# Optimization experiments

Hardware: AMD Instinct MI355X
Metric: run time of the kernel (lower is better)

## Reference

```python
import jax, jax.numpy as jnp
import numpy as np

N_NODES = 25000
N_EDGES = 300000
B = 25            # graphs in the batch
NPG = N_NODES // B
D = 128           # hidden_dim == out_dim
H = 8             # num_heads
HD = D // H
L = 4             # num_layers
VOCAB = 30000
N_ETYPE = 8


def setup_inputs() -> dict:
    key = jax.random.key(0)
    ks = jax.random.split(key, 16)
    s = 0.05
    # graph structure: edges kept within each graph
    eg = jax.random.randint(ks[0], (N_EDGES,), 0, B)
    src = eg * NPG + jax.random.randint(ks[1], (N_EDGES,), 0, NPG)
    dst = eg * NPG + jax.random.randint(ks[2], (N_EDGES,), 0, NPG)
    tokens = jax.random.randint(ks[3], (N_NODES,), 0, VOCAB)
    etype = jax.random.randint(ks[4], (N_EDGES,), 0, N_ETYPE)
    graph_id = jnp.arange(N_NODES) // NPG
    return {
        "emb_h": jax.random.normal(ks[5], (VOCAB, D)) * s,
        "emb_e": jax.random.normal(ks[6], (N_ETYPE, D)) * s,
        # per-layer stacked params: Q,K,V,proj_e weights (bias=False)
        "w_qkve": jax.random.normal(ks[7], (L, 4, D, D)) * s,
        # output projections O_h, O_e
        "o_w": jax.random.normal(ks[8], (L, 2, D, D)) * s,
        "o_b": jnp.zeros((L, 2, D)),
        # layernorms: [ln1_h, ln1_e, ln2_h, ln2_e]
        "ln_scale": jnp.ones((L, 4, D)),
        "ln_bias": jnp.zeros((L, 4, D)),
        # FFNs for h and e: D -> 2D -> D
        "ffn_w1": jax.random.normal(ks[9], (L, 2, D, 2 * D)) * s,
        "ffn_b1": jnp.zeros((L, 2, 2 * D)),
        "ffn_w2": jax.random.normal(ks[10], (L, 2, 2 * D, D)) * s,
        "ffn_b2": jnp.zeros((L, 2, D)),
        # MLPReadout (L=2): 128 -> 64 -> 32 -> 1
        "mlp_w0": jax.random.normal(ks[11], (D, D // 2)) * s,
        "mlp_b0": jnp.zeros((D // 2,)),
        "mlp_w1": jax.random.normal(ks[12], (D // 2, D // 4)) * s,
        "mlp_b1": jnp.zeros((D // 4,)),
        "mlp_w2": jax.random.normal(ks[13], (D // 4, 1)) * s,
        "mlp_b2": jnp.zeros((1,)),
        "tokens": tokens,
        "etype": etype,
        "src": src,
        "dst": dst,
        "graph_id": graph_id,
    }


def _ln(x, g, b):
    m = jnp.mean(x, axis=-1, keepdims=True)
    v = jnp.mean(jnp.square(x - m), axis=-1, keepdims=True)
    return g * (x - m) / jnp.sqrt(v + 1e-5) + b


def _layer(h, e, src, dst, wq, wk, wv, we, o_w, o_b, ln_s, ln_b,
           ffn_w1, ffn_b1, ffn_w2, ffn_b2):
    n = h.shape[0]
    Q = (h @ wq).reshape(n, H, HD)
    K = (h @ wk).reshape(n, H, HD)
    V = (h @ wv).reshape(n, H, HD)
    pe = (e @ we).reshape(-1, H, HD)
    # per-edge implicit attention: (K_src * Q_dst)/sqrt(d) * proj_e
    score = (K[src] * Q[dst]) / jnp.sqrt(jnp.asarray(HD, h.dtype)) * pe  # [E,H,HD]
    e_att = score.reshape(-1, D)
    w = jnp.exp(jnp.clip(jnp.sum(score, axis=-1, keepdims=True), -5.0, 5.0))  # [E,H,1]
    wV = jax.ops.segment_sum((V[src] * w).reshape(-1, D), dst, num_segments=n)
    z = jax.ops.segment_sum(w[:, :, 0], dst, num_segments=n)  # [N,H]
    h_att = (wV.reshape(n, H, HD) / (z[:, :, None] + 1e-6)).reshape(n, D)
    # O proj + residual + LN
    h1 = _ln(h + (h_att @ o_w[0] + o_b[0]), ln_s[0], ln_b[0])
    e1 = _ln(e + (e_att @ o_w[1] + o_b[1]), ln_s[1], ln_b[1])
    # FFNs + residual + LN
    h2 = _ln(h1 + jax.nn.relu(h1 @ ffn_w1[0] + ffn_b1[0]) @ ffn_w2[0] + ffn_b2[0],
             ln_s[2], ln_b[2])
    e2 = _ln(e1 + jax.nn.relu(e1 @ ffn_w1[1] + ffn_b1[1]) @ ffn_w2[1] + ffn_b2[1],
             ln_s[3], ln_b[3])
    return h2, e2


def reference(emb_h, emb_e, w_qkve, o_w, o_b, ln_scale, ln_bias,
              ffn_w1, ffn_b1, ffn_w2, ffn_b2,
              mlp_w0, mlp_b0, mlp_w1, mlp_b1, mlp_w2, mlp_b2,
              tokens, etype, src, dst, graph_id):
    h = emb_h[tokens]   # [N,D]
    e = emb_e[etype]    # [E,D]
    for l in range(L):
        h, e = _layer(h, e, src, dst,
                      w_qkve[l, 0], w_qkve[l, 1], w_qkve[l, 2], w_qkve[l, 3],
                      o_w[l], o_b[l], ln_scale[l], ln_bias[l],
                      ffn_w1[l], ffn_b1[l], ffn_w2[l], ffn_b2[l])
    # mean-nodes readout per graph
    hg_sum = jax.ops.segment_sum(h, graph_id, num_segments=B)
    cnt = jax.ops.segment_sum(jnp.ones((h.shape[0], 1), h.dtype), graph_id, num_segments=B)
    hg = hg_sum / cnt
    # MLPReadout
    y = jax.nn.relu(hg @ mlp_w0 + mlp_b0)
    y = jax.nn.relu(y @ mlp_w1 + mlp_b1)
    return y @ mlp_w2 + mlp_b2  # [B,1]
```

## Files before the change

### kernel.cpp

```cpp
#include <hip/hip_runtime.h>
#include <cstdint>

#define NN 25000
#define NE 300000

typedef unsigned short ushort_t;
typedef __attribute__((ext_vector_type(8))) short bf16x8;
typedef __attribute__((ext_vector_type(4))) float f32x4;
typedef __attribute__((ext_vector_type(4))) unsigned short u16x4;
typedef __attribute__((ext_vector_type(8))) unsigned short u16x8;

__device__ __forceinline__ float4 ld4(const float* p){ return *reinterpret_cast<const float4*>(p); }
__device__ __forceinline__ void st4(float* p, const float4& v){ *reinterpret_cast<float4*>(p) = v; }
__device__ __forceinline__ float bf2f(ushort_t u){ return __uint_as_float((unsigned)u << 16); }
__device__ __forceinline__ ushort_t f2bfu(float f){
  unsigned x = __float_as_uint(f);
  return (ushort_t)((x + 0x7fffu + ((x >> 16) & 1u)) >> 16);
}

#define FXS 4294967296.0
#define FXI 2.3283064365386963e-10
__device__ __forceinline__ long long f2fx(float v) {
  return (long long)llrint((double)v * FXS);
}
__device__ __forceinline__ float fx2f(long long q) { return (float)((double)q * FXI); }

#define MFMA(a, b, c) __builtin_amdgcn_mfma_f32_16x16x32_bf16((a), (b), (c), 0, 0, 0)

__global__ __launch_bounds__(256)
void wconv_k(const float* __restrict__ src, ushort_t* __restrict__ dst,
             int K, int N, int total)
{
  int i = blockIdx.x * 256 + threadIdx.x;
  if (i >= total) return;
  int kn = K * N;
  int mat = i / kn, r = i - mat * kn;
  int n = r / K, k = r - n * K;
  dst[i] = f2bfu(src[(size_t)mat * kn + (size_t)k * N + n]);
}

__global__ __launch_bounds__(256)
void gather_h_k(const float* __restrict__ tab, const int* __restrict__ idx,
                float* __restrict__ hf, ushort_t* __restrict__ hb)
{
  int t = blockIdx.x * 256 + threadIdx.x;
  if (t >= NN * 32) return;
  int i = t >> 5, c4 = t & 31;
  float4 v = ld4(tab + (size_t)idx[i] * 128 + c4 * 4);
  st4(hf + (size_t)i * 128 + c4 * 4, v);
  u16x4 b = { f2bfu(v.x), f2bfu(v.y), f2bfu(v.z), f2bfu(v.w) };
  *reinterpret_cast<u16x4*>(hb + (size_t)i * 128 + c4 * 4) = b;
}

__global__ __launch_bounds__(256)
void gather_e_k(const float* __restrict__ tab, const int* __restrict__ idx,
                ushort_t* __restrict__ eb)
{
  int t = blockIdx.x * 256 + threadIdx.x;
  if (t >= NE * 32) return;
  int i = t >> 5, c4 = t & 31;
  float4 v = ld4(tab + (size_t)idx[i] * 128 + c4 * 4);
  u16x4 b = { f2bfu(v.x), f2bfu(v.y), f2bfu(v.z), f2bfu(v.w) };
  *reinterpret_cast<u16x4*>(eb + (size_t)i * 128 + c4 * 4) = b;
}

__global__ __launch_bounds__(256)
void count_k(const int* __restrict__ dst, int* __restrict__ counts)
{
  int e = blockIdx.x * 256 + threadIdx.x;
  if (e < NE) atomicAdd(&counts[dst[e]], 1);
}

__global__ __launch_bounds__(1024)
void scan_k(const int* __restrict__ counts, int* __restrict__ start,
            int* __restrict__ cursor)
{
  __shared__ int part[1024];
  const int t = threadIdx.x;
  const int base = t * 25;
  int loc[25];
  int s = 0;
#pragma unroll
  for (int i = 0; i < 25; ++i) {
    int n = base + i;
    int c = (n < NN) ? counts[n] : 0;
    loc[i] = s; s += c;
  }
  part[t] = s;
  __syncthreads();
  for (int off = 1; off < 1024; off <<= 1) {
    int v = (t >= off) ? part[t - off] : 0;
    __syncthreads();
    part[t] += v;
    __syncthreads();
  }
  int excl = (t == 0) ? 0 : part[t - 1];
#pragma unroll
  for (int i = 0; i < 25; ++i) {
    int n = base + i;
    if (n < NN) { int v = excl + loc[i]; start[n] = v; cursor[n] = v; }
  }
  if (t == 0) start[NN] = NE;
}

__global__ __launch_bounds__(256)
void scatter_k(const int* __restrict__ src, const int* __restrict__ dst,
               int* __restrict__ cursor, int2* __restrict__ csr_es)
{
  int e = blockIdx.x * 256 + threadIdx.x;
  if (e >= NE) return;
  int pos = atomicAdd(&cursor[dst[e]], 1);
  csr_es[pos] = make_int2(e, src[e]);
}

__global__ __launch_bounds__(256)
void gemmN_bf_k(const ushort_t* __restrict__ A, const ushort_t* __restrict__ WT,
                const int K, const int M, const int ldo,
                const float* __restrict__ Bias, const int osep,
                const float* __restrict__ ResF, const ushort_t* __restrict__ ResB,
                const float* __restrict__ G, const float* __restrict__ Bb,
                ushort_t* __restrict__ OutB, float* __restrict__ OutF)
{
  __shared__ __align__(16) ushort_t SM[2 * 128 * 136];
  __shared__ float mu[128], rs[128];
  ushort_t* Xs = SM;
  ushort_t* Ws = SM + 128 * 136;
  const int tid = threadIdx.x;
  const int m0 = blockIdx.x * 128;
  const int col0 = blockIdx.y * 128;

  const int l = tid & 63, wv = tid >> 6;
  const int lr = l & 15, lk = l >> 4;
  const int mb = (wv & 1) * 64, nb = (wv >> 1) * 64;
  f32x4 acc[4][4];
  const f32x4 zf = {0.f, 0.f, 0.f, 0.f};
#pragma unroll
  for (int mi = 0; mi < 4; ++mi)
#pragma unroll
    for (int ni = 0; ni < 4; ++ni) acc[mi][ni] = zf;

  for (int kc = 0; kc < K; kc += 128) {
    if (kc) __syncthreads();
    for (int c = tid; c < 2048; c += 256) {
      int r = c >> 4, k8 = c & 15;
      bf16x8 v = {};
      if (m0 + r < M)
        v = *reinterpret_cast<const bf16x8*>(A + (size_t)(m0 + r) * K + kc + k8 * 8);
      *reinterpret_cast<bf16x8*>(Xs + r * 136 + k8 * 8) = v;
    }
    for (int c = tid; c < 2048; c += 256) {
      int r = c >> 4, k8 = c & 15;
      *reinterpret_cast<bf16x8*>(Ws + r * 136 + k8 * 8) =
          *reinterpret_cast<const bf16x8*>(WT + (size_t)(col0 + r) * K + kc + k8 * 8);
    }
    __syncthreads();
#pragma unroll
    for (int kt = 0; kt < 4; ++kt) {
      bf16x8 af[4], bw[4];
#pragma unroll
      for (int i = 0; i < 4; ++i)
        af[i] = *reinterpret_cast<const bf16x8*>(Xs + (mb + i * 16 + lr) * 136 + kt * 32 + lk * 8);
#pragma unroll
      for (int i = 0; i < 4; ++i)
        bw[i] = *reinterpret_cast<const bf16x8*>(Ws + (nb + i * 16 + lr) * 136 + kt * 32 + lk * 8);
#pragma unroll
      for (int mi = 0; mi < 4; ++mi)
#pragma unroll
        for (int ni = 0; ni < 4; ++ni)
          acc[mi][ni] = MFMA(af[mi], bw[ni], acc[mi][ni]);
    }
  }

  if (G == nullptr) {
    __syncthreads();
    ushort_t* Rb = SM;
#pragma unroll
    for (int mi = 0; mi < 4; ++mi)
#pragma unroll
      for (int rr = 0; rr < 4; ++rr) {
        int row = mb + mi * 16 + lk * 4 + rr;
#pragma unroll
        for (int ni = 0; ni < 4; ++ni) {
          int col = nb + ni * 16 + lr;
          float v = acc[mi][ni][rr];
          if (Bias) v = fmaxf(v + Bias[col0 + col], 0.f);
          Rb[row * 136 + col] = f2bfu(v);
        }
      }
    __syncthreads();
    ushort_t* ob = OutB + (osep ? (size_t)blockIdx.y * M * 128 : (size_t)col0);
    for (int c = tid; c < 2048; c += 256) {
      int r = c >> 4, k8 = c & 15;
      if (m0 + r < M)
        *reinterpret_cast<u16x8*>(ob + (size_t)(m0 + r) * ldo + k8 * 8) =
            *reinterpret_cast<u16x8*>(Rb + r * 136 + k8 * 8);
    }
    return;
  }

  __syncthreads();
  float* Tf = reinterpret_cast<float*>(SM);
#pragma unroll
  for (int mi = 0; mi < 4; ++mi)
#pragma unroll
    for (int rr = 0; rr < 4; ++rr) {
      int row = mb + mi * 16 + lk * 4 + rr;
      int grow = m0 + row;
#pragma unroll
      for (int ni = 0; ni < 4; ++ni) {
        int col = nb + ni * 16 + lr;
        float t = acc[mi][ni][rr] + Bias[col];
        if (grow < M)
          t += ResF ? ResF[(size_t)grow * 128 + col] : bf2f(ResB[(size_t)grow * 128 + col]);
        Tf[row * 132 + col] = t;
      }
    }
  __syncthreads();
  {
    int r = tid >> 1, jj = tid & 1;
    const float* tp = Tf + r * 132 + jj * 64;
    float s = 0.f;
    for (int c2 = 0; c2 < 64; ++c2) s += tp[c2];
    s += __shfl_xor(s, 1);
    float mean = s * (1.f / 128.f);
    float v = 0.f;
    for (int c2 = 0; c2 < 64; ++c2) { float d = tp[c2] - mean; v += d * d; }
    v += __shfl_xor(v, 1);
    if (jj == 0) { mu[r] = mean; rs[r] = 1.f / sqrtf(v * (1.f / 128.f) + 1e-5f); }
  }
  __syncthreads();
  for (int c = tid; c < 4096; c += 256) {
    int r = c >> 5, c4 = c & 31;
    int grow = m0 + r;
    if (grow >= M) continue;
    float4 t = ld4(Tf + r * 132 + c4 * 4);
    float4 gv = ld4(G + c4 * 4), bv = ld4(Bb + c4 * 4);
    float m = mu[r], ir = rs[r];
    float o0 = gv.x * (t.x - m) * ir + bv.x;
    float o1 = gv.y * (t.y - m) * ir + bv.y;
    float o2 = gv.z * (t.z - m) * ir + bv.z;
    float o3 = gv.w * (t.w - m) * ir + bv.w;
    u16x4 ub = { f2bfu(o0), f2bfu(o1), f2bfu(o2), f2bfu(o3) };
    *reinterpret_cast<u16x4*>(OutB + (size_t)grow * 128 + c4 * 4) = ub;
    if (OutF) st4(OutF + (size_t)grow * 128 + c4 * 4, make_float4(o0, o1, o2, o3));
  }
}

__global__ __launch_bounds__(256)
void ffn_f_k(const ushort_t* __restrict__ Xbf, const float* __restrict__ ResF,
             const ushort_t* __restrict__ W1T, const float* __restrict__ B1,
             const ushort_t* __restrict__ W2T, const float* __restrict__ B2,
             const float* __restrict__ G, const float* __restrict__ Bb,
             ushort_t* __restrict__ OutB, float* __restrict__ OutF, int M)
{
  __shared__ __align__(16) ushort_t SM[8704 + 8704 + 17408];
  __shared__ float mu[64], rs[64];
  ushort_t* Xs   = SM;
  ushort_t* Mid0 = SM + 8704;
  ushort_t* Wst  = SM + 17408;
  const int tid = threadIdx.x;
  const int m0 = blockIdx.x * 64;
  const int l = tid & 63, wv = tid >> 6, lr = l & 15, lk = l >> 4;
  const f32x4 zf = {0.f, 0.f, 0.f, 0.f};

  for (int c = tid; c < 1024; c += 256) {
    int r = c >> 4, k8 = c & 15;
    bf16x8 v = {};
    if (m0 + r < M) v = *reinterpret_cast<const bf16x8*>(Xbf + (size_t)(m0 + r) * 128 + k8 * 8);
    *reinterpret_cast<bf16x8*>(Xs + r * 136 + k8 * 8) = v;
  }
  for (int c = tid; c < 2048; c += 256) {
    int r = c >> 4, k8 = c & 15;
    *reinterpret_cast<bf16x8*>(Wst + r * 136 + k8 * 8) =
        *reinterpret_cast<const bf16x8*>(W1T + (size_t)r * 128 + k8 * 8);
  }
  __syncthreads();

  f32x4 acc2[8];
#pragma unroll
  for (int i = 0; i < 8; ++i) acc2[i] = zf;
  ushort_t rsv[8][4];

  {
    f32x4 a1[8];
#pragma unroll
    for (int i = 0; i < 8; ++i) a1[i] = zf;
#pragma unroll
    for (int kt = 0; kt < 4; ++kt) {
      bf16x8 af = *reinterpret_cast<const bf16x8*>(Xs + (wv * 16 + lr) * 136 + kt * 32 + lk * 8);
#pragma unroll
      for (int ni = 0; ni < 8; ++ni) {
        bf16x8 bw = *reinterpret_cast<const bf16x8*>(Wst + (ni * 16 + lr) * 136 + kt * 32 + lk * 8);
        a1[ni] = MFMA(af, bw, a1[ni]);
      }
    }
#pragma unroll
    for (int ni = 0; ni < 8; ++ni)
#pragma unroll
      for (int rr = 0; rr < 4; ++rr)
        Mid0[(wv * 16 + lk * 4 + rr) * 136 + ni * 16 + lr] =
            f2bfu(fmaxf(a1[ni][rr] + B1[ni * 16 + lr], 0.f));
  }
  __syncthreads();
  for (int c = tid; c < 2048; c += 256) {
    int r = c >> 4, k8 = c & 15;
    *reinterpret_cast<bf16x8*>(Wst + r * 136 + k8 * 8) =
        *reinterpret_cast<const bf16x8*>(W1T + (size_t)(128 + r) * 128 + k8 * 8);
  }
  __syncthreads();
  {
    f32x4 a1[8];
#pragma unroll
    for (int i = 0; i < 8; ++i) a1[i] = zf;
#pragma unroll
    for (int kt = 0; kt < 4; ++kt) {
      bf16x8 af = *reinterpret_cast<const bf16x8*>(Xs + (wv * 16 + lr) * 136 + kt * 32 + lk * 8);
#pragma unroll
      for (int ni = 0; ni < 8; ++ni) {
        bf16x8 bw = *reinterpret_cast<const bf16x8*>(Wst + (ni * 16 + lr) * 136 + kt * 32 + lk * 8);
        a1[ni] = MFMA(af, bw, a1[ni]);
      }
    }
    __syncthreads();
    if (!ResF) {
#pragma unroll
      for (int ni = 0; ni < 8; ++ni)
#pragma unroll
        for (int rr = 0; rr < 4; ++rr)
          rsv[ni][rr] = Xs[(wv * 16 + lk * 4 + rr) * 136 + ni * 16 + lr];
    }
#pragma unroll
    for (int ni = 0; ni < 8; ++ni)
#pragma unroll
      for (int rr = 0; rr < 4; ++rr)
        Xs[(wv * 16 + lk * 4 + rr) * 136 + ni * 16 + lr] =
            f2bfu(fmaxf(a1[ni][rr] + B1[128 + ni * 16 + lr], 0.f));
  }
  __syncthreads();
  for (int c = tid; c < 2048; c += 256) {
    int r = c >> 4, k8 = c & 15;
    *reinterpret_cast<bf16x8*>(Wst + r * 136 + k8 * 8) =
        *reinterpret_cast<const bf16x8*>(W2T + (size_t)r * 256 + k8 * 8);
  }
  __syncthreads();
#pragma unroll
  for (int kt = 0; kt < 4; ++kt) {
    bf16x8 af = *reinterpret_cast<const bf16x8*>(Mid0 + (wv * 16 + lr) * 136 + kt * 32 + lk * 8);
#pragma unroll
    for (int ni = 0; ni < 8; ++ni) {
      bf16x8 bw = *reinterpret_cast<const bf16x8*>(Wst + (ni * 16 + lr) * 136 + kt * 32 + lk * 8);
      acc2[ni] = MFMA(af, bw, acc2[ni]);
    }
  }
  __syncthreads();
  for (int c = tid; c < 2048; c += 256) {
    int r = c >> 4, k8 = c & 15;
    *reinterpret_cast<bf16x8*>(Wst + r * 136 + k8 * 8) =
        *reinterpret_cast<const bf16x8*>(W2T + (size_t)r * 256 + 128 + k8 * 8);
  }
  __syncthreads();
#pragma unroll
  for (int kt = 0; kt < 4; ++kt) {
    bf16x8 af = *reinterpret_cast<const bf16x8*>(Xs + (wv * 16 + lr) * 136 + kt * 32 + lk * 8);
#pragma unroll
    for (int ni = 0; ni < 8; ++ni) {
      bf16x8 bw = *reinterpret_cast<const bf16x8*>(Wst + (ni * 16 + lr) * 136 + kt * 32 + lk * 8);
      acc2[ni] = MFMA(af, bw, acc2[ni]);
    }
  }
  __syncthreads();
  float* Tf = reinterpret_cast<float*>(Wst);
#pragma unroll
  for (int ni = 0; ni < 8; ++ni)
#pragma unroll
    for (int rr = 0; rr < 4; ++rr) {
      int row = wv * 16 + lk * 4 + rr;
      int grow = m0 + row;
      int col = ni * 16 + lr;
      float t = acc2[ni][rr] + B2[col];
      if (ResF) { if (grow < M) t += ResF[(size_t)grow * 128 + col]; }
      else      t += bf2f(rsv[ni][rr]);
      Tf[row * 132 + col] = t;
    }
  __syncthreads();
  {
    int r = tid >> 2, jj = tid & 3;
    const float* tp = Tf + r * 132 + jj * 32;
    float s = 0.f;
    for (int c2 = 0; c2 < 32; ++c2) s += tp[c2];
    s += __shfl_xor(s, 1); s += __shfl_xor(s, 2);
    float mean = s * (1.f / 128.f);
    float v = 0.f;
    for (int c2 = 0; c2 < 32; ++c2) { float d = tp[c2] - mean; v += d * d; }
    v += __shfl_xor(v, 1); v += __shfl_xor(v, 2);
    if (jj == 0) { mu[r] = mean; rs[r] = 1.f / sqrtf(v * (1.f / 128.f) + 1e-5f); }
  }
  __syncthreads();
  for (int c = tid; c < 2048; c += 256) {
    int r = c >> 5, c4 = c & 31;
    int grow = m0 + r;
    if (grow >= M) continue;
    float4 t = ld4(Tf + r * 132 + c4 * 4);
    float4 gv = ld4(G + c4 * 4), bv = ld4(Bb + c4 * 4);
    float m = mu[r], ir = rs[r];
    float o0 = gv.x * (t.x - m) * ir + bv.x;
    float o1 = gv.y * (t.y - m) * ir + bv.y;
    float o2 = gv.z * (t.z - m) * ir + bv.z;
    float o3 = gv.w * (t.w - m) * ir + bv.w;
    u16x4 ub = { f2bfu(o0), f2bfu(o1), f2bfu(o2), f2bfu(o3) };
    *reinterpret_cast<u16x4*>(OutB + (size_t)grow * 128 + c4 * 4) = ub;
    if (OutF) st4(OutF + (size_t)grow * 128 + c4 * 4, make_float4(o0, o1, o2, o3));
  }
}

__global__ __launch_bounds__(256)
void efused_k(ushort_t* __restrict__ Ebuf,
              const ushort_t* __restrict__ Qb, const ushort_t* __restrict__ Kb,
              const int* __restrict__ src, const int* __restrict__ dst,
              float* __restrict__ wbuf,
              const ushort_t* __restrict__ weT,
              const ushort_t* __restrict__ owT, const float* __restrict__ oBias,
              const float* __restrict__ G1, const float* __restrict__ B1n,
              const ushort_t* __restrict__ W1T, const float* __restrict__ fB1,
              const ushort_t* __restrict__ W2T, const float* __restrict__ fB2,
              const float* __restrict__ G2, const float* __restrict__ B2n,
              int M)
{
  __shared__ __align__(16) ushort_t SM[34816];
  __shared__ float mu[64], rs[64];
  ushort_t* Es   = SM;
  ushort_t* Mid0 = SM + 8704;
  ushort_t* Wst  = SM + 17408;
  const int tid = threadIdx.x;
  const int m0 = blockIdx.x * 64;
  const int l = tid & 63, wv = tid >> 6, lr = l & 15, lk = l >> 4;
  const f32x4 zf = {0.f, 0.f, 0.f, 0.f};

  for (int c = tid; c < 1024; c += 256) {
    int r = c >> 4, k8 = c & 15;
    bf16x8 v = {};
    if (m0 + r < M) v = *reinterpret_cast<const bf16x8*>(Ebuf + (size_t)(m0 + r) * 128 + k8 * 8);
    *reinterpret_cast<bf16x8*>(Es + r * 136 + k8 * 8) = v;
  }
  for (int c = tid; c < 2048; c += 256) {
    int r = c >> 4, k8 = c & 15;
    *reinterpret_cast<bf16x8*>(Wst + r * 136 + k8 * 8) =
        *reinterpret_cast<const bf16x8*>(weT + (size_t)r * 128 + k8 * 8);
  }
  __syncthreads();

  {
    f32x4 a1[8];
#pragma unroll
    for (int i = 0; i < 8; ++i) a1[i] = zf;
#pragma unroll
    for (int kt = 0; kt < 4; ++kt) {
      bf16x8 af = *reinterpret_cast<const bf16x8*>(Es + (wv * 16 + lr) * 136 + kt * 32 + lk * 8);
#pragma unroll
      for (int ni = 0; ni < 8; ++ni) {
        bf16x8 bw = *reinterpret_cast<const bf16x8*>(Wst + (ni * 16 + lr) * 136 + kt * 32 + lk * 8);
        a1[ni] = MFMA(af, bw, a1[ni]);
      }
    }
#pragma unroll
    for (int ni = 0; ni < 8; ++ni)
#pragma unroll
      for (int rr = 0; rr < 4; ++rr)
        Mid0[(wv * 16 + lk * 4 + rr) * 136 + ni * 16 + lr] = f2bfu(a1[ni][rr]);
  }
  __syncthreads();

  for (int c = tid; c < 1024; c += 256) {
    int r = c >> 4, j = c & 15;
    int e = m0 + r;
    if (e < M) {
      int s = src[e], d = dst[e];
      u16x8 kv = *reinterpret_cast<const u16x8*>(Kb + (size_t)s * 128 + j * 8);
      u16x8 qv = *reinterpret_cast<const u16x8*>(Qb + (size_t)d * 128 + j * 8);
      u16x8 pv = *reinterpret_cast<const u16x8*>(Mid0 + r * 136 + j * 8);
      float hsum = 0.f;
      u16x8 ob;
#pragma unroll
      for (int i = 0; i < 8; ++i) {
        float x = bf2f(kv[i]) * bf2f(qv[i]) * 0.25f * bf2f(pv[i]);
        hsum += x; ob[i] = f2bfu(x);
      }
      *reinterpret_cast<u16x8*>(Mid0 + r * 136 + j * 8) = ob;
      hsum += __shfl_xor(hsum, 1);
      float w = expf(fminf(fmaxf(hsum, -5.f), 5.f));
      if ((j & 1) == 0) wbuf[(size_t)e * 8 + (j >> 1)] = w;
    }
  }
  __syncthreads();

  for (int c = tid; c < 2048; c += 256) {
    int r = c >> 4, k8 = c & 15;
    *reinterpret_cast<bf16x8*>(Wst + r * 136 + k8 * 8) =
        *reinterpret_cast<const bf16x8*>(owT + (size_t)r * 128 + k8 * 8);
  }
  __syncthreads();

  {
    f32x4 a1[8];
#pragma unroll
    for (int i = 0; i < 8; ++i) a1[i] = zf;
#pragma unroll
    for (int kt = 0; kt < 4; ++kt) {
      bf16x8 af = *reinterpret_cast<const bf16x8*>(Mid0 + (wv * 16 + lr) * 136 + kt * 32 + lk * 8);
#pragma unroll
      for (int ni = 0; ni < 8; ++ni) {
        bf16x8 bw = *reinterpret_cast<const bf16x8*>(Wst + (ni * 16 + lr) * 136 + kt * 32 + lk * 8);
        a1[ni] = MFMA(af, bw, a1[ni]);
      }
    }
    __syncthreads();
    float* Tf = reinterpret_cast<float*>(Wst);
#pragma unroll
    for (int ni = 0; ni < 8; ++ni)
#pragma unroll
      for (int rr = 0; rr < 4; ++rr) {
        int row = wv * 16 + lk * 4 + rr;
        int col = ni * 16 + lr;
        Tf[row * 132 + col] = a1[ni][rr] + oBias[col] + bf2f(Es[row * 136 + col]);
      }
  }
  __syncthreads();
  {
    float* Tf = reinterpret_cast<float*>(Wst);
    int r = tid >> 2, jj = tid & 3;
    const float* tp = Tf + r * 132 + jj * 32;
    float s = 0.f;
    for (int c2 = 0; c2 < 32; ++c2) s += tp[c2];
    s += __shfl_xor(s, 1); s += __shfl_xor(s, 2);
    float mean = s * (1.f / 128.f);
    float v = 0.f;
    for (int c2 = 0; c2 < 32; ++c2) { float d = tp[c2] - mean; v += d * d; }
    v += __shfl_xor(v, 1); v += __shfl_xor(v, 2);
    if (jj == 0) { mu[r] = mean; rs[r] = 1.f / sqrtf(v * (1.f / 128.f) + 1e-5f); }
  }
  __syncthreads();
  {
    float* Tf = reinterpret_cast<float*>(Wst);
    for (int c = tid; c < 2048; c += 256) {
      int r = c >> 5, c4 = c & 31;
      float4 t = ld4(Tf + r * 132 + c4 * 4);
      float4 gv = ld4(G1 + c4 * 4), bv = ld4(B1n + c4 * 4);
      float m = mu[r], ir = rs[r];
      u16x4 ub = { f2bfu(gv.x * (t.x - m) * ir + bv.x), f2bfu(gv.y * (t.y - m) * ir + bv.y),
                   f2bfu(gv.z * (t.z - m) * ir + bv.z), f2bfu(gv.w * (t.w - m) * ir + bv.w) };
      *reinterpret_cast<u16x4*>(Es + r * 136 + c4 * 4) = ub;
    }
  }
  __syncthreads();

  f32x4 acc2[8];
#pragma unroll
  for (int i = 0; i < 8; ++i) acc2[i] = zf;
  ushort_t rsv[8][4];

  for (int c = tid; c < 2048; c += 256) {
    int r = c >> 4, k8 = c & 15;
    *reinterpret_cast<bf16x8*>(Wst + r * 136 + k8 * 8) =
        *reinterpret_cast<const bf16x8*>(W1T + (size_t)r * 128 + k8 * 8);
  }
  __syncthreads();
  {
    f32x4 a1[8];
#pragma unroll
    for (int i = 0; i < 8; ++i) a1[i] = zf;
#pragma unroll
    for (int kt = 0; kt < 4; ++kt) {
      bf16x8 af = *reinterpret_cast<const bf16x8*>(Es + (wv * 16 + lr) * 136 + kt * 32 + lk * 8);
#pragma unroll
      for (int ni = 0; ni < 8; ++ni) {
        bf16x8 bw = *reinterpret_cast<const bf16x8*>(Wst + (ni * 16 + lr) * 136 + kt * 32 + lk * 8);
        a1[ni] = MFMA(af, bw, a1[ni]);
      }
    }
    __syncthreads();
#pragma unroll
    for (int ni = 0; ni < 8; ++ni)
#pragma unroll
      for (int rr = 0; rr < 4; ++rr)
        Mid0[(wv * 16 + lk * 4 + rr) * 136 + ni * 16 + lr] =
            f2bfu(fmaxf(a1[ni][rr] + fB1[ni * 16 + lr], 0.f));
  }
  __syncthreads();
  for (int c = tid; c < 2048; c += 256) {
    int r = c >> 4, k8 = c & 15;
    *reinterpret_cast<bf16x8*>(Wst + r * 136 + k8 * 8) =
        *reinterpret_cast<const bf16x8*>(W1T + (size_t)(128 + r) * 128 + k8 * 8);
  }
  __syncthreads();
  {
    f32x4 a1[8];
#pragma unroll
    for (int i = 0; i < 8; ++i) a1[i] = zf;
#pragma unroll
    for (int kt = 0; kt < 4; ++kt) {
      bf16x8 af = *reinterpret_cast<const bf16x8*>(Es + (wv * 16 + lr) * 136 + kt * 32 + lk * 8);
#pragma unroll
      for (int ni = 0; ni < 8; ++ni) {
        bf16x8 bw = *reinterpret_cast<const bf16x8*>(Wst + (ni * 16 + lr) * 136 + kt * 32 + lk * 8);
        a1[ni] = MFMA(af, bw, a1[ni]);
      }
    }
    __syncthreads();
#pragma unroll
    for (int ni = 0; ni < 8; ++ni)
#pragma unroll
      for (int rr = 0; rr < 4; ++rr)
        rsv[ni][rr] = Es[(wv * 16 + lk * 4 + rr) * 136 + ni * 16 + lr];
#pragma unroll
    for (int ni = 0; ni < 8; ++ni)
#pragma unroll
      for (int rr = 0; rr < 4; ++rr)
        Es[(wv * 16 + lk * 4 + rr) * 136 + ni * 16 + lr] =
            f2bfu(fmaxf(a1[ni][rr] + fB1[128 + ni * 16 + lr], 0.f));
  }
  __syncthreads();
  for (int c = tid; c < 2048; c += 256) {
    int r = c >> 4, k8 = c & 15;
    *reinterpret_cast<bf16x8*>(Wst + r * 136 + k8 * 8) =
        *reinterpret_cast<const bf16x8*>(W2T + (size_t)r * 256 + k8 * 8);
  }
  __syncthreads();
#pragma unroll
  for (int kt = 0; kt < 4; ++kt) {
    bf16x8 af = *reinterpret_cast<const bf16x8*>(Mid0 + (wv * 16 + lr) * 136 + kt * 32 + lk * 8);
#pragma unroll
    for (int ni = 0; ni < 8; ++ni) {
      bf16x8 bw = *reinterpret_cast<const bf16x8*>(Wst + (ni * 16 + lr) * 136 + kt * 32 + lk * 8);
      acc2[ni] = MFMA(af, bw, acc2[ni]);
    }
  }
  __syncthreads();
  for (int c = tid; c < 2048; c += 256) {
    int r = c >> 4, k8 = c & 15;
    *reinterpret_cast<bf16x8*>(Wst + r * 136 + k8 * 8) =
        *reinterpret_cast<const bf16x8*>(W2T + (size_t)r * 256 + 128 + k8 * 8);
  }
  __syncthreads();
#pragma unroll
  for (int kt = 0; kt < 4; ++kt) {
    bf16x8 af = *reinterpret_cast<const bf16x8*>(Es + (wv * 16 + lr) * 136 + kt * 32 + lk * 8);
#pragma unroll
    for (int ni = 0; ni < 8; ++ni) {
      bf16x8 bw = *reinterpret_cast<const bf16x8*>(Wst + (ni * 16 + lr) * 136 + kt * 32 + lk * 8);
      acc2[ni] = MFMA(af, bw, acc2[ni]);
    }
  }
  __syncthreads();
  float* Tf = reinterpret_cast<float*>(Wst);
#pragma unroll
  for (int ni = 0; ni < 8; ++ni)
#pragma unroll
    for (int rr = 0; rr < 4; ++rr) {
      int row = wv * 16 + lk * 4 + rr;
      int col = ni * 16 + lr;
      Tf[row * 132 + col] = acc2[ni][rr] + fB2[col] + bf2f(rsv[ni][rr]);
    }
  __syncthreads();
  {
    int r = tid >> 2, jj = tid & 3;
    const float* tp = Tf + r * 132 + jj * 32;
    float s = 0.f;
    for (int c2 = 0; c2 < 32; ++c2) s += tp[c2];
    s += __shfl_xor(s, 1); s += __shfl_xor(s, 2);
    float mean = s * (1.f / 128.f);
    float v = 0.f;
    for (int c2 = 0; c2 < 32; ++c2) { float d = tp[c2] - mean; v += d * d; }
    v += __shfl_xor(v, 1); v += __shfl_xor(v, 2);
    if (jj == 0) { mu[r] = mean; rs[r] = 1.f / sqrtf(v * (1.f / 128.f) + 1e-5f); }
  }
  __syncthreads();
  for (int c = tid; c < 2048; c += 256) {
    int r = c >> 5, c4 = c & 31;
    int grow = m0 + r;
    if (grow >= M) continue;
    float4 t = ld4(Tf + r * 132 + c4 * 4);
    float4 gv = ld4(G2 + c4 * 4), bv = ld4(B2n + c4 * 4);
    float m = mu[r], ir = rs[r];
    u16x4 ub = { f2bfu(gv.x * (t.x - m) * ir + bv.x), f2bfu(gv.y * (t.y - m) * ir + bv.y),
                 f2bfu(gv.z * (t.z - m) * ir + bv.z), f2bfu(gv.w * (t.w - m) * ir + bv.w) };
    *reinterpret_cast<u16x4*>(Ebuf + (size_t)grow * 128 + c4 * 4) = ub;
  }
}

__global__ __launch_bounds__(256)
void reduce_k(const ushort_t* __restrict__ V, const float* __restrict__ wbuf,
              const int* __restrict__ start, const int2* __restrict__ csr_es,
              ushort_t* __restrict__ out)
{
  int t = blockIdx.x * 256 + threadIdx.x;
  int n = t >> 4;
  if (n >= NN) return;
  int j = t & 15;
  int p0 = start[n], p1 = start[n + 1];
  long long acc[8] = {};
  long long zacc = 0;
  for (int p = p0; p < p1; ++p) {
    int2 es = csr_es[p];
    float w = wbuf[(size_t)es.x * 8 + (j >> 1)];
    u16x8 vv = *reinterpret_cast<const u16x8*>(V + (size_t)es.y * 128 + j * 8);
    zacc += f2fx(w);
#pragma unroll
    for (int i = 0; i < 8; ++i) acc[i] += f2fx(bf2f(vv[i]) * w);
  }
  float zz = fx2f(zacc) + 1e-6f;
  u16x8 ob;
#pragma unroll
  for (int i = 0; i < 8; ++i) ob[i] = f2bfu(fx2f(acc[i]) / zz);
  *reinterpret_cast<u16x8*>(out + (size_t)n * 128 + j * 8) = ob;
}

__global__ __launch_bounds__(256)
void graphmean_k(const float* __restrict__ h, float* __restrict__ hg)
{
  __shared__ float red[256];
  int g = blockIdx.x, tid = threadIdx.x;
  int c = tid & 127, half = tid >> 7;
  float s = 0.f;
  for (int r = half; r < 1000; r += 2) s += h[(size_t)(g * 1000 + r) * 128 + c];
  red[tid] = s;
  __syncthreads();
  if (half == 0) hg[g * 128 + c] = (red[c] + red[c + 128]) / 1000.0f;
}

__global__ __launch_bounds__(256)
void readout_k(const float* __restrict__ hg,
               const float* __restrict__ w0, const float* __restrict__ b0,
               const float* __restrict__ w1, const float* __restrict__ b1,
               const float* __restrict__ w2, const float* __restrict__ b2,
               float* __restrict__ out)
{
  __shared__ float hs[25 * 128];
  __shared__ float t0[25 * 64];
  __shared__ float t1[25 * 32];
  int tid = threadIdx.x;
  for (int i = tid; i < 25 * 128; i += 256) hs[i] = hg[i];
  __syncthreads();
  for (int i = tid; i < 25 * 64; i += 256) {
    int r = i >> 6, c = i & 63;
    float a = b0[c];
    for (int k = 0; k < 128; k++) a += hs[r * 128 + k] * w0[k * 64 + c];
    t0[i] = fmaxf(a, 0.f);
  }
  __syncthreads();
  for (int i = tid; i < 25 * 32; i += 256) {
    int r = i >> 5, c = i & 31;
    float a = b1[c];
    for (int k = 0; k < 64; k++) a += t0[r * 64 + k] * w1[k * 32 + c];
    t1[i] = fmaxf(a, 0.f);
  }
  __syncthreads();
  if (tid < 25) {
    float a = b2[0];
    for (int k = 0; k < 32; k++) a += t1[tid * 32 + k] * w2[k];
    out[tid] = a;
  }
}

extern "C" void kernel_launch(void* const* d_in, const int* in_sizes, int n_in,
                              void* d_out, int out_size, void* d_ws, size_t ws_size,
                              hipStream_t stream)
{
  const float* emb_h  = (const float*)d_in[0];
  const float* emb_e  = (const float*)d_in[1];
  const float* w_qkve = (const float*)d_in[2];
  const float* o_w    = (const float*)d_in[3];
  const float* o_b    = (const float*)d_in[4];
  const float* ln_s   = (const float*)d_in[5];
  const float* ln_b   = (const float*)d_in[6];
  const float* ffn_w1 = (const float*)d_in[7];
  const float* ffn_b1 = (const float*)d_in[8];
  const float* ffn_w2 = (const float*)d_in[9];
  const float* ffn_b2 = (const float*)d_in[10];
  const float* mlp_w0 = (const float*)d_in[11];
  const float* mlp_b0 = (const float*)d_in[12];
  const float* mlp_w1 = (const float*)d_in[13];
  const float* mlp_b1 = (const float*)d_in[14];
  const float* mlp_w2 = (const float*)d_in[15];
  const float* mlp_b2 = (const float*)d_in[16];
  const int* tokens = (const int*)d_in[17];
  const int* etype  = (const int*)d_in[18];
  const int* src    = (const int*)d_in[19];
  const int* dst    = (const int*)d_in[20];

  char* ws = (char*)d_ws;
  size_t off = 0;
  auto alloc = [&](size_t bytes) { char* p = ws + off; off += bytes; return p; };
  int2*      csr_es = (int2*)alloc((size_t)NE * 8);
  float*     h      = (float*)alloc((size_t)NN * 128 * 4);
  float*     hg     = (float*)alloc(25 * 128 * 4);
  float*     wbuf   = (float*)alloc((size_t)NE * 8 * 4);
  int*       counts = (int*)alloc((size_t)NN * 4);
  int*       cursor = (int*)alloc((size_t)NN * 4);
  int*       startp = (int*)alloc((size_t)(NN + 1) * 4);
  ushort_t*  h_bf   = (ushort_t*)alloc((size_t)NN * 128 * 2);
  ushort_t*  ha_bf  = (ushort_t*)alloc((size_t)NN * 128 * 2);
  ushort_t*  Qb     = (ushort_t*)alloc((size_t)NN * 128 * 2);
  ushort_t*  Kb     = (ushort_t*)alloc((size_t)NN * 128 * 2);
  ushort_t*  Vb     = (ushort_t*)alloc((size_t)NN * 128 * 2);
  ushort_t*  e_bf   = (ushort_t*)alloc((size_t)NE * 128 * 2);
  ushort_t*  wt     = (ushort_t*)alloc(917504 * 2);

  ushort_t* qkveT = wt;
  ushort_t* owT   = wt + 262144;
  ushort_t* w1T   = wt + 393216;
  ushort_t* w2T   = wt + 655360;
  wconv_k<<<1024, 256, 0, stream>>>(w_qkve, qkveT, 128, 128, 262144);
  wconv_k<<<512,  256, 0, stream>>>(o_w,    owT,   128, 128, 131072);
  wconv_k<<<1024, 256, 0, stream>>>(ffn_w1, w1T,   128, 256, 262144);
  wconv_k<<<1024, 256, 0, stream>>>(ffn_w2, w2T,   256, 128, 262144);

  gather_h_k<<<3125, 256, 0, stream>>>(emb_h, tokens, h, h_bf);
  gather_e_k<<<37500, 256, 0, stream>>>(emb_e, etype, e_bf);

  hipMemsetAsync(counts, 0, (size_t)NN * 4, stream);
  count_k<<<(NE + 255) / 256, 256, 0, stream>>>(dst, counts);
  scan_k<<<1, 1024, 0, stream>>>(counts, startp, cursor);
  scatter_k<<<(NE + 255) / 256, 256, 0, stream>>>(src, dst, cursor, csr_es);

  const int GN = (NN + 127) / 128;
  const int FN = (NN + 63) / 64;
  const int FE = (NE + 63) / 64;

  for (int l = 0; l < 4; ++l) {
    const ushort_t* qkvT = qkveT + (size_t)l * 4 * 16384;
    const ushort_t* weT  = qkveT + ((size_t)l * 4 + 3) * 16384;
    const ushort_t* ow0T = owT + ((size_t)l * 2 + 0) * 16384;
    const ushort_t* ow1T = owT + ((size_t)l * 2 + 1) * 16384;
    const ushort_t* w1hT = w1T + ((size_t)l * 2 + 0) * 32768;
    const ushort_t* w1eT = w1T + ((size_t)l * 2 + 1) * 32768;
    const ushort_t* w2hT = w2T + ((size_t)l * 2 + 0) * 32768;
    const ushort_t* w2eT = w2T + ((size_t)l * 2 + 1) * 32768;
    const float* ob0 = o_b + ((size_t)l * 2 + 0) * 128;
    const float* ob1 = o_b + ((size_t)l * 2 + 1) * 128;
    const float* ls0 = ln_s + ((size_t)l * 4 + 0) * 128;
    const float* ls1 = ln_s + ((size_t)l * 4 + 1) * 128;
    const float* ls2 = ln_s + ((size_t)l * 4 + 2) * 128;
    const float* ls3 = ln_s + ((size_t)l * 4 + 3) * 128;
    const float* lb0 = ln_b + ((size_t)l * 4 + 0) * 128;
    const float* lb1 = ln_b + ((size_t)l * 4 + 1) * 128;
    const float* lb2 = ln_b + ((size_t)l * 4 + 2) * 128;
    const float* lb3 = ln_b + ((size_t)l * 4 + 3) * 128;
    const float* fb1h = ffn_b1 + ((size_t)l * 2 + 0) * 256;
    const float* fb1e = ffn_b1 + ((size_t)l * 2 + 1) * 256;
    const float* fb2h = ffn_b2 + ((size_t)l * 2 + 0) * 128;
    const float* fb2e = ffn_b2 + ((size_t)l * 2 + 1) * 128;

    gemmN_bf_k<<<dim3(GN, 3), 256, 0, stream>>>(h_bf, qkvT, 128, NN, 128,
        nullptr, 1, nullptr, nullptr, nullptr, nullptr, Qb, nullptr);

    efused_k<<<FE, 256, 0, stream>>>(e_bf, Qb, Kb, src, dst, wbuf,
        weT, ow1T, ob1, ls1, lb1, w1eT, fb1e, w2eT, fb2e, ls3, lb3, NE);

    reduce_k<<<1563, 256, 0, stream>>>(Vb, wbuf, startp, csr_es, ha_bf);
    gemmN_bf_k<<<dim3(GN, 1), 256, 0, stream>>>(ha_bf, ow0T, 128, NN, 128,
        ob0, 0, h, nullptr, ls0, lb0, h_bf, h);
    ffn_f_k<<<FN, 256, 0, stream>>>(h_bf, h, w1hT, fb1h, w2hT, fb2h,
                                    ls2, lb2, h_bf, h, NN);
  }

  graphmean_k<<<25, 256, 0, stream>>>(h, hg);
  readout_k<<<1, 256, 0, stream>>>(hg, mlp_w0, mlp_b0, mlp_w1, mlp_b1, mlp_w2, mlp_b2,
                                   (float*)d_out);
}
```

Measured before the change: 1.822 ms.

## Make edge-fused kernel wave-private: read weights from global, in-register layernorm, drop barriers

Restructures the fused edge kernel so each wave works only on its own 16 rows. Weight tiles are read directly from global or L2 instead of being staged in shared memory. LayerNorm is computed in registers with 16-lane shuffles instead of through a float scratch tile, and almost all __syncthreads are removed. Shared memory drops from about 70KB to 35KB, which should raise occupancy. The cost is that every wave now reloads the B fragments from global memory, adding cache traffic and latency on the MFMA inner loops.

```diff
diff --git a/kernel.cpp b/kernel.cpp
--- a/kernel.cpp
+++ b/kernel.cpp
@@ -16,6 +16,11 @@
 __device__ __forceinline__ ushort_t f2bfu(float f){
   unsigned x = __float_as_uint(f);
   return (ushort_t)((x + 0x7fffu + ((x >> 16) & 1u)) >> 16);
+}
+__device__ __forceinline__ float rsum16(float s) {
+  s += __shfl_xor(s, 1); s += __shfl_xor(s, 2);
+  s += __shfl_xor(s, 4); s += __shfl_xor(s, 8);
+  return s;
 }
 
 #define FXS 4294967296.0
@@ -426,15 +431,14 @@
               const float* __restrict__ G2, const float* __restrict__ B2n,
               int M)
 {
-  __shared__ __align__(16) ushort_t SM[34816];
-  __shared__ float mu[64], rs[64];
-  ushort_t* Es   = SM;
-  ushort_t* Mid0 = SM + 8704;
-  ushort_t* Wst  = SM + 17408;
+  __shared__ __align__(16) ushort_t Es[64 * 136];
+  __shared__ __align__(16) ushort_t Mid0[64 * 136];
   const int tid = threadIdx.x;
   const int m0 = blockIdx.x * 64;
   const int l = tid & 63, wv = tid >> 6, lr = l & 15, lk = l >> 4;
   const f32x4 zf = {0.f, 0.f, 0.f, 0.f};
+  const int arow = (wv * 16 + lr) * 136;
+  const int orow0 = (wv * 16 + lk * 4) * 136;
 
   for (int c = tid; c < 1024; c += 256) {
     int r = c >> 4, k8 = c & 15;
@@ -442,11 +446,6 @@
     if (m0 + r < M) v = *reinterpret_cast<const bf16x8*>(Ebuf + (size_t)(m0 + r) * 128 + k8 * 8);
     *reinterpret_cast<bf16x8*>(Es + r * 136 + k8 * 8) = v;
   }
-  for (int c = tid; c < 2048; c += 256) {
-    int r = c >> 4, k8 = c & 15;
-    *reinterpret_cast<bf16x8*>(Wst + r * 136 + k8 * 8) =
-        *reinterpret_cast<const bf16x8*>(weT + (size_t)r * 128 + k8 * 8);
-  }
   __syncthreads();
 
   {
@@ -455,10 +454,10 @@
     for (int i = 0; i < 8; ++i) a1[i] = zf;
 #pragma unroll
     for (int kt = 0; kt < 4; ++kt) {
-      bf16x8 af = *reinterpret_cast<const bf16x8*>(Es + (wv * 16 + lr) * 136 + kt * 32 + lk * 8);
+      bf16x8 af = *reinterpret_cast<const bf16x8*>(Es + arow + kt * 32 + lk * 8);
 #pragma unroll
       for (int ni = 0; ni < 8; ++ni) {
-        bf16x8 bw = *reinterpret_cast<const bf16x8*>(Wst + (ni * 16 + lr) * 136 + kt * 32 + lk * 8);
+        bf16x8 bw = *reinterpret_cast<const bf16x8*>(weT + (size_t)(ni * 16 + lr) * 128 + kt * 32 + lk * 8);
         a1[ni] = MFMA(af, bw, a1[ni]);
       }
     }
@@ -466,14 +465,15 @@
     for (int ni = 0; ni < 8; ++ni)
 #pragma unroll
       for (int rr = 0; rr < 4; ++rr)
-        Mid0[(wv * 16 + lk * 4 + rr) * 136 + ni * 16 + lr] = f2bfu(a1[ni][rr]);
-  }
-  __syncthreads();
-
-  for (int c = tid; c < 1024; c += 256) {
-    int r = c >> 4, j = c & 15;
+        Mid0[orow0 + rr * 136 + ni * 16 + lr] = f2bfu(a1[ni][rr]);
+  }
+
+#pragma unroll
+  for (int it = 0; it < 4; ++it) {
+    int r = wv * 16 + it * 4 + lk;
     int e = m0 + r;
     if (e < M) {
+      int j = lr;
       int s = src[e], d = dst[e];
       u16x8 kv = *reinterpret_cast<const u16x8*>(Kb + (size_t)s * 128 + j * 8);
       u16x8 qv = *reinterpret_cast<const u16x8*>(Qb + (size_t)d * 128 + j * 8);
@@ -491,14 +491,6 @@
       if ((j & 1) == 0) wbuf[(size_t)e * 8 + (j >> 1)] = w;
     }
   }
-  __syncthreads();
-
-  for (int c = tid; c < 2048; c += 256) {
-    int r = c >> 4, k8 = c & 15;
-    *reinterpret_cast<bf16x8*>(Wst + r * 136 + k8 * 8) =
-        *reinterpret_cast<const bf16x8*>(owT + (size_t)r * 128 + k8 * 8);
-  }
-  __syncthreads();
 
   {
     f32x4 a1[8];
@@ -506,184 +498,141 @@
     for (int i = 0; i < 8; ++i) a1[i] = zf;
 #pragma unroll
     for (int kt = 0; kt < 4; ++kt) {
-      bf16x8 af = *reinterpret_cast<const bf16x8*>(Mid0 + (wv * 16 + lr) * 136 + kt * 32 + lk * 8);
+      bf16x8 af = *reinterpret_cast<const bf16x8*>(Mid0 + arow + kt * 32 + lk * 8);
 #pragma unroll
       for (int ni = 0; ni < 8; ++ni) {
-        bf16x8 bw = *reinterpret_cast<const bf16x8*>(Wst + (ni * 16 + lr) * 136 + kt * 32 + lk * 8);
+        bf16x8 bw = *reinterpret_cast<const bf16x8*>(owT + (size_t)(ni * 16 + lr) * 128 + kt * 32 + lk * 8);
         a1[ni] = MFMA(af, bw, a1[ni]);
       }
     }
-    __syncthreads();
-    float* Tf = reinterpret_cast<float*>(Wst);
-#pragma unroll
-    for (int ni = 0; ni < 8; ++ni)
-#pragma unroll
-      for (int rr = 0; rr < 4; ++rr) {
-        int row = wv * 16 + lk * 4 + rr;
+    float t[8][4];
+#pragma unroll
+    for (int ni = 0; ni < 8; ++ni) {
+      int col = ni * 16 + lr;
+      float bb = oBias[col];
+#pragma unroll
+      for (int rr = 0; rr < 4; ++rr)
+        t[ni][rr] = a1[ni][rr] + bb + bf2f(Es[orow0 + rr * 136 + col]);
+    }
+#pragma unroll
+    for (int rr = 0; rr < 4; ++rr) {
+      float s = 0.f;
+#pragma unroll
+      for (int ni = 0; ni < 8; ++ni) s += t[ni][rr];
+      float mean = rsum16(s) * (1.f / 128.f);
+      float v = 0.f;
+#pragma unroll
+      for (int ni = 0; ni < 8; ++ni) { float d = t[ni][rr] - mean; v += d * d; }
+      float ir = 1.f / sqrtf(rsum16(v) * (1.f / 128.f) + 1e-5f);
+#pragma unroll
+      for (int ni = 0; ni < 8; ++ni) {
         int col = ni * 16 + lr;
-        Tf[row * 132 + col] = a1[ni][rr] + oBias[col] + bf2f(Es[row * 136 + col]);
-      }
-  }
-  __syncthreads();
-  {
-    float* Tf = reinterpret_cast<float*>(Wst);
-    int r = tid >> 2, jj = tid & 3;
-    const float* tp = Tf + r * 132 + jj * 32;
-    float s = 0.f;
-    for (int c2 = 0; c2 < 32; ++c2) s += tp[c2];
-    s += __shfl_xor(s, 1); s += __shfl_xor(s, 2);
-    float mean = s * (1.f / 128.f);
-    float v = 0.f;
-    for (int c2 = 0; c2 < 32; ++c2) { float d = tp[c2] - mean; v += d * d; }
-    v += __shfl_xor(v, 1); v += __shfl_xor(v, 2);
-    if (jj == 0) { mu[r] = mean; rs[r] = 1.f / sqrtf(v * (1.f / 128.f) + 1e-5f); }
-  }
-  __syncthreads();
-  {
-    float* Tf = reinterpret_cast<float*>(Wst);
-    for (int c = tid; c < 2048; c += 256) {
-      int r = c >> 5, c4 = c & 31;
-      float4 t = ld4(Tf + r * 132 + c4 * 4);
-      float4 gv = ld4(G1 + c4 * 4), bv = ld4(B1n + c4 * 4);
-      float m = mu[r], ir = rs[r];
-      u16x4 ub = { f2bfu(gv.x * (t.x - m) * ir + bv.x), f2bfu(gv.y * (t.y - m) * ir + bv.y),
-                   f2bfu(gv.z * (t.z - m) * ir + bv.z), f2bfu(gv.w * (t.w - m) * ir + bv.w) };
-      *reinterpret_cast<u16x4*>(Es + r * 136 + c4 * 4) = ub;
-    }
-  }
-  __syncthreads();
-
-  f32x4 acc2[8];
-#pragma unroll
-  for (int i = 0; i < 8; ++i) acc2[i] = zf;
-  ushort_t rsv[8][4];
-
-  for (int c = tid; c < 2048; c += 256) {
-    int r = c >> 4, k8 = c & 15;
-    *reinterpret_cast<bf16x8*>(Wst + r * 136 + k8 * 8) =
-        *reinterpret_cast<const bf16x8*>(W1T + (size_t)r * 128 + k8 * 8);
-  }
-  __syncthreads();
+        Es[orow0 + rr * 136 + col] =
+            f2bfu(G1[col] * (t[ni][rr] - mean) * ir + B1n[col]);
+      }
+    }
+  }
+
   {
     f32x4 a1[8];
 #pragma unroll
     for (int i = 0; i < 8; ++i) a1[i] = zf;
 #pragma unroll
     for (int kt = 0; kt < 4; ++kt) {
-      bf16x8 af = *reinterpret_cast<const bf16x8*>(Es + (wv * 16 + lr) * 136 + kt * 32 + lk * 8);
+      bf16x8 af = *reinterpret_cast<const bf16x8*>(Es + arow + kt * 32 + lk * 8);
 #pragma unroll
       for (int ni = 0; ni < 8; ++ni) {
-        bf16x8 bw = *reinterpret_cast<const bf16x8*>(Wst + (ni * 16 + lr) * 136 + kt * 32 + lk * 8);
+        bf16x8 bw = *reinterpret_cast<const bf16x8*>(W1T + (size_t)(ni * 16 + lr) * 128 + kt * 32 + lk * 8);
         a1[ni] = MFMA(af, bw, a1[ni]);
       }
     }
-    __syncthreads();
 #pragma unroll
     for (int ni = 0; ni < 8; ++ni)
 #pragma unroll
       for (int rr = 0; rr < 4; ++rr)
-        Mid0[(wv * 16 + lk * 4 + rr) * 136 + ni * 16 + lr] =
+        Mid0[orow0 + rr * 136 + ni * 16 + lr] =
             f2bfu(fmaxf(a1[ni][rr] + fB1[ni * 16 + lr], 0.f));
   }
-  __syncthreads();
-  for (int c = tid; c < 2048; c += 256) {
-    int r = c >> 4, k8 = c & 15;
-    *reinterpret_cast<bf16x8*>(Wst + r * 136 + k8 * 8) =
-        *reinterpret_cast<const bf16x8*>(W1T + (size_t)(128 + r) * 128 + k8 * 8);
-  }
-  __syncthreads();
+
+  f32x4 acc2[8];
+#pragma unroll
+  for (int i = 0; i < 8; ++i) acc2[i] = zf;
+
+#pragma unroll
+  for (int kt = 0; kt < 4; ++kt) {
+    bf16x8 af = *reinterpret_cast<const bf16x8*>(Mid0 + arow + kt * 32 + lk * 8);
+#pragma unroll
+    for (int ni = 0; ni < 8; ++ni) {
+      bf16x8 bw = *reinterpret_cast<const bf16x8*>(W2T + (size_t)(ni * 16 + lr) * 256 + kt * 32 + lk * 8);
+      acc2[ni] = MFMA(af, bw, acc2[ni]);
+    }
+  }
+
   {
     f32x4 a1[8];
 #pragma unroll
     for (int i = 0; i < 8; ++i) a1[i] = zf;
 #pragma unroll
     for (int kt = 0; kt < 4; ++kt) {
-      bf16x8 af = *reinterpret_cast<const bf16x8*>(Es + (wv * 16 + lr) * 136 + kt * 32 + lk * 8);
+      bf16x8 af = *reinterpret_cast<const bf16x8*>(Es + arow + kt * 32 + lk * 8);
 #pragma unroll
       for (int ni = 0; ni < 8; ++ni) {
-        bf16x8 bw = *reinterpret_cast<const bf16x8*>(Wst + (ni * 16 + lr) * 136 + kt * 32 + lk * 8);
+        bf16x8 bw = *reinterpret_cast<const bf16x8*>(W1T + (size_t)(128 + ni * 16 + lr) * 128 + kt * 32 + lk * 8);
         a1[ni] = MFMA(af, bw, a1[ni]);
       }
     }
-    __syncthreads();
 #pragma unroll
     for (int ni = 0; ni < 8; ++ni)
 #pragma unroll
       for (int rr = 0; rr < 4; ++rr)
-        rsv[ni][rr] = Es[(wv * 16 + lk * 4 + rr) * 136 + ni * 16 + lr];
-#pragma unroll
-    for (int ni = 0; ni < 8; ++ni)
+        Mid0[orow0 + rr * 136 + ni * 16 + lr] =
+            f2bfu(fmaxf(a1[ni][rr] + fB1[128 + ni * 16 + lr], 0.f));
+  }
+
+#pragma unroll
+  for (int kt = 0; kt < 4; ++kt) {
+    bf16x8 af = *reinterpret_cast<const bf16x8*>(Mid0 + arow + kt * 32 + lk * 8);
+#pragma unroll
+    for (int ni = 0; ni < 8; ++ni) {
+      bf16x8 bw = *reinterpret_cast<const bf16x8*>(W2T + (size_t)(ni * 16 + lr) * 256 + 128 + kt * 32 + lk * 8);
+      acc2[ni] = MFMA(af, bw, acc2[ni]);
+    }
+  }
+
+  {
+    float t[8][4];
+#pragma unroll
+    for (int ni = 0; ni < 8; ++ni) {
+      int col = ni * 16 + lr;
+      float bb = fB2[col];
 #pragma unroll
       for (int rr = 0; rr < 4; ++rr)
-        Es[(wv * 16 + lk * 4 + rr) * 136 + ni * 16 + lr] =
-            f2bfu(fmaxf(a1[ni][rr] + fB1[128 + ni * 16 + lr], 0.f));
-  }
-  __syncthreads();
-  for (int c = tid; c < 2048; c += 256) {
-    int r = c >> 4, k8 = c & 15;
-    *reinterpret_cast<bf16x8*>(Wst + r * 136 + k8 * 8) =
-        *reinterpret_cast<const bf16x8*>(W2T + (size_t)r * 256 + k8 * 8);
-  }
-  __syncthreads();
-#pragma unroll
-  for (int kt = 0; kt < 4; ++kt) {
-    bf16x8 af = *reinterpret_cast<const bf16x8*>(Mid0 + (wv * 16 + lr) * 136 + kt * 32 + lk * 8);
-#pragma unroll
-    for (int ni = 0; ni < 8; ++ni) {
-      bf16x8 bw = *reinterpret_cast<const bf16x8*>(Wst + (ni * 16 + lr) * 136 + kt * 32 + lk * 8);
-      acc2[ni] = MFMA(af, bw, acc2[ni]);
-    }
-  }
-  __syncthreads();
-  for (int c = tid; c < 2048; c += 256) {
-    int r = c >> 4, k8 = c & 15;
-    *reinterpret_cast<bf16x8*>(Wst + r * 136 + k8 * 8) =
-        *reinterpret_cast<const bf16x8*>(W2T + (size_t)r * 256 + 128 + k8 * 8);
-  }
-  __syncthreads();
-#pragma unroll
-  for (int kt = 0; kt < 4; ++kt) {
-    bf16x8 af = *reinterpret_cast<const bf16x8*>(Es + (wv * 16 + lr) * 136 + kt * 32 + lk * 8);
-#pragma unroll
-    for (int ni = 0; ni < 8; ++ni) {
-      bf16x8 bw = *reinterpret_cast<const bf16x8*>(Wst + (ni * 16 + lr) * 136 + kt * 32 + lk * 8);
-      acc2[ni] = MFMA(af, bw, acc2[ni]);
-    }
-  }
-  __syncthreads();
-  float* Tf = reinterpret_cast<float*>(Wst);
-#pragma unroll
-  for (int ni = 0; ni < 8; ++ni)
+        t[ni][rr] = acc2[ni][rr] + bb + bf2f(Es[orow0 + rr * 136 + col]);
+    }
 #pragma unroll
     for (int rr = 0; rr < 4; ++rr) {
-      int row = wv * 16 + lk * 4 + rr;
-      int col = ni * 16 + lr;
-      Tf[row * 132 + col] = acc2[ni][rr] + fB2[col] + bf2f(rsv[ni][rr]);
-    }
-  __syncthreads();
-  {
-    int r = tid >> 2, jj = tid & 3;
-    const float* tp = Tf + r * 132 + jj * 32;
-    float s = 0.f;
-    for (int c2 = 0; c2 < 32; ++c2) s += tp[c2];
-    s += __shfl_xor(s, 1); s += __shfl_xor(s, 2);
-    float mean = s * (1.f / 128.f);
-    float v = 0.f;
-    for (int c2 = 0; c2 < 32; ++c2) { float d = tp[c2] - mean; v += d * d; }
-    v += __shfl_xor(v, 1); v += __shfl_xor(v, 2);
-    if (jj == 0) { mu[r] = mean; rs[r] = 1.f / sqrtf(v * (1.f / 128.f) + 1e-5f); }
-  }
-  __syncthreads();
-  for (int c = tid; c < 2048; c += 256) {
-    int r = c >> 5, c4 = c & 31;
-    int grow = m0 + r;
-    if (grow >= M) continue;
-    float4 t = ld4(Tf + r * 132 + c4 * 4);
-    float4 gv = ld4(G2 + c4 * 4), bv = ld4(B2n + c4 * 4);
-    float m = mu[r], ir = rs[r];
-    u16x4 ub = { f2bfu(gv.x * (t.x - m) * ir + bv.x), f2bfu(gv.y * (t.y - m) * ir + bv.y),
-                 f2bfu(gv.z * (t.z - m) * ir + bv.z), f2bfu(gv.w * (t.w - m) * ir + bv.w) };
-    *reinterpret_cast<u16x4*>(Ebuf + (size_t)grow * 128 + c4 * 4) = ub;
+      float s = 0.f;
+#pragma unroll
+      for (int ni = 0; ni < 8; ++ni) s += t[ni][rr];
+      float mean = rsum16(s) * (1.f / 128.f);
+      float v = 0.f;
+#pragma unroll
+      for (int ni = 0; ni < 8; ++ni) { float d = t[ni][rr] - mean; v += d * d; }
+      float ir = 1.f / sqrtf(rsum16(v) * (1.f / 128.f) + 1e-5f);
+#pragma unroll
+      for (int ni = 0; ni < 8; ++ni) {
+        int col = ni * 16 + lr;
+        Mid0[orow0 + rr * 136 + col] =
+            f2bfu(G2[col] * (t[ni][rr] - mean) * ir + B2n[col]);
+      }
+    }
+#pragma unroll
+    for (int it = 0; it < 4; ++it) {
+      int r = wv * 16 + it * 4 + lk;
+      if (m0 + r < M)
+        *reinterpret_cast<u16x8*>(Ebuf + (size_t)(m0 + r) * 128 + lr * 8) =
+            *reinterpret_cast<u16x8*>(Mid0 + r * 136 + lr * 8);
+    }
   }
 }
 
```

Result: slower. 2.621 ms (+43.9%).
